# Optimization experiments

Hardware: AMD Instinct MI355X
Metric: run time of the kernel (lower is better)

## Reference

```python
import jax, jax.numpy as jnp
import numpy as np

M = 16384      # total flat points per role (8 scenes x 2048 pts)
D = 256        # d_model
H = 4          # heads
K = 16         # knn neighbors
DFF = 1024     # 4*D
LN_EPS = 1e-5


def _ln(x, g, b):
    m = jnp.mean(x, axis=-1, keepdims=True)
    v = jnp.mean((x - m) ** 2, axis=-1, keepdims=True)
    return (x - m) / jnp.sqrt(v + LN_EPS) * g + b


def _knn_block(x, coord, ctx, ctx_coord, idx,
               Wq, Wk, Wv, Wo, g1, b1, pe_w, pe_b,
               W1, bf1, W2, bf2, g2, b2):
    # x: [M,D] query feats; ctx: [N,D] context feats; idx: [M,K] neighbor ids (-1 = invalid)
    m, d = x.shape
    k = idx.shape[1]
    dh = d // H
    valid = idx >= 0
    idx_c = jnp.where(valid, idx, 0)

    xn = _ln(x, g1, b1)
    q = (xn @ Wq).reshape(m, H, dh)                      # [M,H,dh]
    k_all = ctx @ Wk                                     # [N,D]
    v_all = ctx @ Wv                                     # [N,D]

    rel = coord[:, None, :] - ctx_coord[idx_c]           # [M,K,3]
    pe = rel @ pe_w + pe_b                               # [M,K,D] relative position encoding
    kg = (k_all[idx_c] + pe).reshape(m, k, H, dh)        # gathered keys  [M,K,H,dh]
    vg = (v_all[idx_c] + pe).reshape(m, k, H, dh)        # gathered values

    scale = jnp.asarray(1.0 / np.sqrt(dh), x.dtype)
    scores = jnp.einsum('mhd,mkhd->mhk', q, kg) * scale
    scores = jnp.where(valid[:, None, :], scores, jnp.asarray(-1e9, x.dtype))
    attn = jax.nn.softmax(scores, axis=-1)
    out = jnp.einsum('mhk,mkhd->mhd', attn, vg).reshape(m, d) @ Wo
    x = x + out
    h = jax.nn.gelu(_ln(x, g2, b2) @ W1 + bf1)
    return x + (h @ W2 + bf2)


def setup_inputs() -> dict:
    key = jax.random.key(0)
    ks = jax.random.split(key, 24)
    s = 0.02
    nblk = 2  # [0]=self(a), [1]=cross(a,b)
    inp = {
        'feat_a': jax.random.normal(ks[0], (M, D), jnp.float32),
        'coord_a': jax.random.normal(ks[1], (M, 3), jnp.float32),
        'feat_b': jax.random.normal(ks[2], (M, D), jnp.float32),
        'coord_b': jax.random.normal(ks[3], (M, 3), jnp.float32),
        'Wq': jax.random.normal(ks[4], (nblk, D, D), jnp.float32) * s,
        'Wk': jax.random.normal(ks[5], (nblk, D, D), jnp.float32) * s,
        'Wv': jax.random.normal(ks[6], (nblk, D, D), jnp.float32) * s,
        'Wo': jax.random.normal(ks[7], (nblk, D, D), jnp.float32) * s,
        'ln1_g': jnp.ones((nblk, D), jnp.float32),
        'ln1_b': jnp.zeros((nblk, D), jnp.float32),
        'pe_w': jax.random.normal(ks[8], (nblk, 3, D), jnp.float32) * s,
        'pe_b': jnp.zeros((nblk, D), jnp.float32),
        'ffn_w1': jax.random.normal(ks[9], (nblk, D, DFF), jnp.float32) * s,
        'ffn_b1': jnp.zeros((nblk, DFF), jnp.float32),
        'ffn_w2': jax.random.normal(ks[10], (nblk, DFF, D), jnp.float32) * s,
        'ffn_b2': jnp.zeros((nblk, D), jnp.float32),
        'ln2_g': jnp.ones((nblk, D), jnp.float32),
        'ln2_b': jnp.zeros((nblk, D), jnp.float32),
        'knn_a2a': jax.random.randint(ks[11], (M, K), 0, M, jnp.int64 if jax.config.jax_enable_x64 else jnp.int32),
        'knn_a2b': jax.random.randint(ks[12], (M, K), 0, M, jnp.int64 if jax.config.jax_enable_x64 else jnp.int32),
    }
    return inp


def reference(feat_a, coord_a, feat_b, coord_b,
              Wq, Wk, Wv, Wo, ln1_g, ln1_b, pe_w, pe_b,
              ffn_w1, ffn_b1, ffn_w2, ffn_b2, ln2_g, ln2_b,
              knn_a2a, knn_a2b):
    def params(i):
        return (Wq[i], Wk[i], Wv[i], Wo[i], ln1_g[i], ln1_b[i], pe_w[i], pe_b[i],
                ffn_w1[i], ffn_b1[i], ffn_w2[i], ffn_b2[i], ln2_g[i], ln2_b[i])
    # layer 'self(a)': feat[a] = block(feat[a], coord[a], knn_indexes['a2a'])
    fa = _knn_block(feat_a, coord_a, feat_a, coord_a, knn_a2a, *params(0))
    # layer 'cross(a,b)': feat[a] = block(query=feat[a], context=feat[b], knn_indexes['a2b'])
    fa = _knn_block(fa, coord_a, feat_b, coord_b, knn_a2b, *params(1))
    return fa
```

## Files before the change

kernel.cpp:

```cpp
#include <hip/hip_runtime.h>
#include <hip/hip_bf16.h>
#include <stdint.h>

#define MM 16384
#define DD 256
#define HH 4
#define KK 16
#define DFF_ 1024

typedef __attribute__((ext_vector_type(8))) short bf16x8;
typedef __attribute__((ext_vector_type(16))) float f32x16;
typedef __attribute__((ext_vector_type(2))) float f32x2;

__device__ __forceinline__ unsigned short f2bf(float f) {
    unsigned u = __builtin_bit_cast(unsigned, f);
    unsigned r = u + 0x7fffu + ((u >> 16) & 1u);
    return (unsigned short)(r >> 16);
}
__device__ __forceinline__ float bf2f(unsigned short h) {
    unsigned u = ((unsigned)h) << 16;
    return __builtin_bit_cast(float, u);
}


__global__ __launch_bounds__(256) void prep_weights(
        const float* __restrict__ Wq, const float* __restrict__ Wk,
        const float* __restrict__ Wv, const float* __restrict__ Wo,
        const float* __restrict__ W1, const float* __restrict__ W2,
        unsigned short* __restrict__ wf) {
    int t = blockIdx.x * blockDim.x + threadIdx.x;
    const float* src; unsigned short* dst;
    int kd, nsrc, rem, blk, e, sect;
    if (t < 131072) { sect = 0; rem = t; blk = rem >> 16; e = rem & 65535;
        src = Wq; dst = wf + blk * 65536; kd = 256; nsrc = 256; }
    else if (t < 262144) { sect = 1; rem = t - 131072; blk = rem >> 16; e = rem & 65535;
        src = Wk; dst = wf + 131072 + blk * 131072; kd = 256; nsrc = 256; }
    else if (t < 393216) { sect = 2; rem = t - 262144; blk = rem >> 16; e = rem & 65535;
        src = Wv; dst = wf + 131072 + blk * 131072; kd = 256; nsrc = 256; }
    else if (t < 524288) { sect = 0; rem = t - 393216; blk = rem >> 16; e = rem & 65535;
        src = Wo; dst = wf + 393216 + blk * 65536; kd = 256; nsrc = 256; }
    else if (t < 1048576) { sect = 0; rem = t - 524288; blk = rem >> 18; e = rem & 262143;
        src = W1; dst = wf + 524288 + blk * 262144; kd = 256; nsrc = 1024; }
    else if (t < 1572864) { sect = 0; rem = t - 1048576; blk = rem >> 18; e = rem & 262143;
        src = W2; dst = wf + 1048576 + blk * 262144; kd = 1024; nsrc = 256; }
    else return;
    int k = e / nsrc;
    int n = e - k * nsrc;
    if (sect == 1) n = (n >> 2) * 8 + (n & 3);
    else if (sect == 2) n = (n >> 2) * 8 + 4 + (n & 3);
    float v = src[(size_t)blk * kd * nsrc + e];
    int off = ((n >> 5) * (kd >> 4) + (k >> 4)) * 512 + (((k >> 3) & 1) * 32 + (n & 31)) * 8 + (k & 7);
    dst[off] = f2bf(v);
}

__global__ __launch_bounds__(256) void ln_to_frag(
        const float* __restrict__ x, const float* __restrict__ g,
        const float* __restrict__ b, unsigned short* __restrict__ out,
        int apply_ln) {
    int wave = threadIdx.x >> 6, lane = threadIdx.x & 63;
    int m = blockIdx.x * 4 + wave;
    const float4 xv = reinterpret_cast<const float4*>(x + (size_t)m * DD)[lane];
    float vals[4] = {xv.x, xv.y, xv.z, xv.w};
    int k0 = lane * 4;
    if (apply_ln) {
        float s = vals[0] + vals[1] + vals[2] + vals[3];
        float sq = vals[0]*vals[0] + vals[1]*vals[1] + vals[2]*vals[2] + vals[3]*vals[3];
        for (int o = 32; o; o >>= 1) { s += __shfl_xor(s, o, 64); sq += __shfl_xor(sq, o, 64); }
        float mean = s * (1.0f / DD);
        float var = sq * (1.0f / DD) - mean * mean;
        float rs = rsqrtf(var + 1e-5f);
        #pragma unroll
        for (int c = 0; c < 4; ++c)
            vals[c] = (vals[c] - mean) * rs * g[k0 + c] + b[k0 + c];
    }
    int chunk = ((m >> 5) * (DD >> 4) + (k0 >> 4)) * 64 + ((k0 >> 3) & 1) * 32 + (m & 31);
    ushort4 o4 = make_ushort4(f2bf(vals[0]), f2bf(vals[1]), f2bf(vals[2]), f2bf(vals[3]));
    *reinterpret_cast<ushort4*>(out + (size_t)chunk * 8 + (k0 & 7)) = o4;
}

constexpr int GOUT_F32 = 0;
constexpr int GOUT_BF16 = 1;
constexpr int GOUT_GELU_FRAG = 2;

template <int KGH>
__device__ __forceinline__ void compute_tile(
        const bf16x8* __restrict__ a0, const bf16x8* __restrict__ a1,
        const bf16x8* __restrict__ b0, const bf16x8* __restrict__ b1,
        f32x16 acc[2][2]) {
    #pragma unroll 4
    for (int g = 0; g < KGH; ++g) {
        bf16x8 av0 = a0[g * 64];
        bf16x8 av1 = a1[g * 64];
        bf16x8 bv0 = b0[g * 64];
        bf16x8 bv1 = b1[g * 64];
        acc[0][0] = __builtin_amdgcn_mfma_f32_32x32x16_bf16(av0, bv0, acc[0][0], 0, 0, 0);
        acc[0][1] = __builtin_amdgcn_mfma_f32_32x32x16_bf16(av0, bv1, acc[0][1], 0, 0, 0);
        acc[1][0] = __builtin_amdgcn_mfma_f32_32x32x16_bf16(av1, bv0, acc[1][0], 0, 0, 0);
        acc[1][1] = __builtin_amdgcn_mfma_f32_32x32x16_bf16(av1, bv1, acc[1][1], 0, 0, 0);
    }
}

template <int KD, int NOUT, int SPLITK, int MODE, bool RESID, bool BIAS>
__global__ __launch_bounds__(SPLITK * 128) void gemm_frag(
        const bf16x8* __restrict__ A, const bf16x8* __restrict__ B,
        void* __restrict__ outp, const float* __restrict__ resid,
        const float* __restrict__ bias, int out_kd) {
    static_assert(MODE != GOUT_GELU_FRAG || SPLITK == 1, "gelu path is 2-wave only");
    constexpr int KG = KD / 16;
    constexpr int KGH = KG / SPLITK;
    __shared__ float lds[SPLITK == 2 ? 2 * 64 * 64 : 2 * 32 * 33];
    int wave = threadIdx.x >> 6, lane = threadIdx.x & 63;
    int mhalf = wave & 1;
    int khalf = (SPLITK == 2) ? (wave >> 1) : 0;
    int m0 = blockIdx.x * 128 + mhalf * 64;
    int n0 = blockIdx.y * 64;
    const bf16x8* a0 = A + ((size_t)(m0 >> 5) * KG + khalf * KGH) * 64 + lane;
    const bf16x8* a1 = a0 + (size_t)KG * 64;
    const bf16x8* b0 = B + ((size_t)(n0 >> 5) * KG + khalf * KGH) * 64 + lane;
    const bf16x8* b1 = b0 + (size_t)KG * 64;
    f32x16 acc[2][2] = {};
    compute_tile<KGH>(a0, a1, b0, b1, acc);
    int col = lane & 31, rq = (lane >> 5) * 4;
    if constexpr (SPLITK == 2) {
        if (khalf == 1) {
            #pragma unroll
            for (int i = 0; i < 2; ++i)
            #pragma unroll
            for (int j = 0; j < 2; ++j)
            #pragma unroll
            for (int r = 0; r < 16; ++r) {
                int row = (r & 3) + 8 * (r >> 2) + rq + i * 32;
                lds[mhalf * 4096 + row * 64 + j * 32 + col] = acc[i][j][r];
            }
        }
        __syncthreads();
        if (khalf == 1) return;
        #pragma unroll
        for (int i = 0; i < 2; ++i)
        #pragma unroll
        for (int j = 0; j < 2; ++j)
        #pragma unroll
        for (int r = 0; r < 16; ++r) {
            int row = (r & 3) + 8 * (r >> 2) + rq + i * 32;
            acc[i][j][r] += lds[mhalf * 4096 + row * 64 + j * 32 + col];
        }
    }
    if constexpr (MODE != GOUT_GELU_FRAG) {
        #pragma unroll
        for (int i = 0; i < 2; ++i)
        #pragma unroll
        for (int j = 0; j < 2; ++j) {
            #pragma unroll
            for (int r = 0; r < 16; ++r) {
                int row = (r & 3) + 8 * (r >> 2) + rq;
                int m = m0 + i * 32 + row;
                int n = n0 + j * 32 + col;
                float v = acc[i][j][r];
                if (BIAS) v += bias[n];
                if (RESID) v += resid[(size_t)m * NOUT + n];
                if (MODE == GOUT_F32) ((float*)outp)[(size_t)m * NOUT + n] = v;
                else ((unsigned short*)outp)[(size_t)m * NOUT + n] = f2bf(v);
            }
        }
    } else {
        float* wlds = &lds[wave * 1056];
        for (int i = 0; i < 2; ++i)
        for (int j = 0; j < 2; ++j) {
            #pragma unroll
            for (int r = 0; r < 16; ++r) {
                int row = (r & 3) + 8 * (r >> 2) + rq;
                int n = n0 + j * 32 + col;
                float v = acc[i][j][r] + bias[n];
                float arg = v * (1.5957691216f + 0.0713548163f * v * v);
                v = v * __frcp_rn(1.0f + __expf(-arg));
                wlds[row * 33 + col] = v;
            }
            #pragma unroll
            for (int it = 0; it < 2; ++it) {
                int task = lane + it * 64;
                int row = task >> 2, cc = task & 3;
                int m = m0 + i * 32 + row;
                int k = n0 + j * 32 + cc * 8;
                float* p = &wlds[row * 33 + cc * 8];
                unsigned short us[8];
                #pragma unroll
                for (int e = 0; e < 8; ++e) us[e] = f2bf(p[e]);
                int chunk = ((m >> 5) * (out_kd >> 4) + (k >> 4)) * 64 + ((k >> 3) & 1) * 32 + (m & 31);
                reinterpret_cast<uint4*>(outp)[chunk] = *reinterpret_cast<uint4*>(us);
            }
        }
    }
}

__global__ __launch_bounds__(256) void gemm_qkv(
        const bf16x8* __restrict__ Aq, const bf16x8* __restrict__ Akv,
        const bf16x8* __restrict__ Bq, const bf16x8* __restrict__ Bkv,
        unsigned short* __restrict__ qout, unsigned char* __restrict__ kvout) {
    constexpr int KG = 16, KGH = 8;
    __shared__ float lds[2 * 64 * 64];
    int wave = threadIdx.x >> 6, lane = threadIdx.x & 63;
    int mhalf = wave & 1, khalf = wave >> 1;
    int y = blockIdx.y;
    bool isQ = y < 4;
    const bf16x8* A = isQ ? Aq : Akv;
    const bf16x8* B = isQ ? Bq : Bkv;
    int n0 = (isQ ? y : y - 4) * 64;
    int m0 = blockIdx.x * 128 + mhalf * 64;
    const bf16x8* a0 = A + ((size_t)(m0 >> 5) * KG + khalf * KGH) * 64 + lane;
    const bf16x8* a1 = a0 + (size_t)KG * 64;
    const bf16x8* b0 = B + ((size_t)(n0 >> 5) * KG + khalf * KGH) * 64 + lane;
    const bf16x8* b1 = b0 + (size_t)KG * 64;
    f32x16 acc[2][2] = {};
    compute_tile<KGH>(a0, a1, b0, b1, acc);
    int col = lane & 31, rq = (lane >> 5) * 4;
    if (khalf == 1) {
        #pragma unroll
        for (int i = 0; i < 2; ++i)
        #pragma unroll
        for (int j = 0; j < 2; ++j)
        #pragma unroll
        for (int r = 0; r < 16; ++r) {
            int row = (r & 3) + 8 * (r >> 2) + rq + i * 32;
            lds[mhalf * 4096 + row * 64 + j * 32 + col] = acc[i][j][r];
        }
    }
    __syncthreads();
    if (khalf == 1) return;
    #pragma unroll
    for (int i = 0; i < 2; ++i)
    #pragma unroll
    for (int j = 0; j < 2; ++j)
    #pragma unroll
    for (int r = 0; r < 16; ++r) {
        int row = (r & 3) + 8 * (r >> 2) + rq;
        int m = m0 + i * 32 + row;
        int n = n0 + j * 32 + col;
        float v = acc[i][j][r] + lds[mhalf * 4096 + (row + i * 32) * 64 + j * 32 + col];
        if (isQ) qout[(size_t)m * 256 + n] = f2bf(v);
        else kvout[(size_t)m * 512 + n] =
            (unsigned char)(__builtin_amdgcn_cvt_pk_fp8_f32(v, v, 0, false) & 0xff);
    }
}

__global__ __launch_bounds__(256) void attn_kernel(
        const unsigned short* __restrict__ q, const unsigned char* __restrict__ kv,
        const float* __restrict__ coord, const float* __restrict__ ctx_coord,
        const int* __restrict__ knn,
        const float* __restrict__ pe_w, const float* __restrict__ pe_b,
        unsigned short* __restrict__ out_frag) {
    int wave = threadIdx.x >> 6, lane = threadIdx.x & 63;
    int m = blockIdx.x * 4 + wave;
    int s = lane & 15;
    int d0 = (lane >> 4) * 64 + s * 4;

    ushort4 qv4 = *reinterpret_cast<const ushort4*>(q + (size_t)m * DD + d0);
    float qx = bf2f(qv4.x), qy = bf2f(qv4.y), qz = bf2f(qv4.z), qw = bf2f(qv4.w);
    float4 pw0 = *reinterpret_cast<const float4*>(pe_w + d0);
    float4 pw1 = *reinterpret_cast<const float4*>(pe_w + DD + d0);
    float4 pw2 = *reinterpret_cast<const float4*>(pe_w + 2 * DD + d0);
    float4 pbv = *reinterpret_cast<const float4*>(pe_b + d0);

    float cx = coord[m * 3], cy = coord[m * 3 + 1], cz = coord[m * 3 + 2];
    int myidx = knn[(size_t)m * KK + s];
    int icm = myidx < 0 ? 0 : myidx;
    float rx = cx - ctx_coord[icm * 3];
    float ry = cy - ctx_coord[icm * 3 + 1];
    float rz = cz - ctx_coord[icm * 3 + 2];

    float t0 = qx * pw0.x + qy * pw0.y + qz * pw0.z + qw * pw0.w;
    float t1 = qx * pw1.x + qy * pw1.y + qz * pw1.z + qw * pw1.w;
    float t2 = qx * pw2.x + qy * pw2.y + qz * pw2.z + qw * pw2.w;
    float t3 = qx * pbv.x + qy * pbv.y + qz * pbv.z + qw * pbv.w;
    #pragma unroll
    for (int o = 1; o < 16; o <<= 1) {
        t0 += __shfl_xor(t0, o, 64);
        t1 += __shfl_xor(t1, o, 64);
        t2 += __shfl_xor(t2, o, 64);
        t3 += __shfl_xor(t3, o, 64);
    }

    float sc_own = 0.0f;
    unsigned vpk[KK];
    #pragma unroll
    for (int j = 0; j < KK; ++j) {
        int ij = __shfl(myidx, j, 64);
        int ic = ij < 0 ? 0 : ij;
        uint2 kvv = *reinterpret_cast<const uint2*>(kv + (size_t)ic * 512 + (d0 >> 2) * 8);
        vpk[j] = kvv.y;
        f32x2 k01 = __builtin_amdgcn_cvt_pk_f32_fp8(kvv.x, false);
        f32x2 k23 = __builtin_amdgcn_cvt_pk_f32_fp8(kvv.x, true);
        float p = qx * k01.x + qy * k01.y + qz * k23.x + qw * k23.y;
        p += __shfl_xor(p, 1, 64);
        p += __shfl_xor(p, 2, 64);
        p += __shfl_xor(p, 4, 64);
        p += __shfl_xor(p, 8, 64);
        sc_own = (j == s) ? p : sc_own;
    }
    float corr = rx * t0 + ry * t1 + rz * t2 + t3;
    sc_own = (myidx >= 0) ? (sc_own + corr) * 0.125f : -1e9f;

    float mx = sc_own;
    mx = fmaxf(mx, __shfl_xor(mx, 1, 64));
    mx = fmaxf(mx, __shfl_xor(mx, 2, 64));
    mx = fmaxf(mx, __shfl_xor(mx, 4, 64));
    mx = fmaxf(mx, __shfl_xor(mx, 8, 64));
    float e = __expf(sc_own - mx);
    float sum = e;
    sum += __shfl_xor(sum, 1, 64);
    sum += __shfl_xor(sum, 2, 64);
    sum += __shfl_xor(sum, 4, 64);
    sum += __shfl_xor(sum, 8, 64);
    float w_own = e * __frcp_rn(sum);

    float wrx = w_own * rx, wry = w_own * ry, wrz = w_own * rz;
    #pragma unroll
    for (int o = 1; o < 16; o <<= 1) {
        wrx += __shfl_xor(wrx, o, 64);
        wry += __shfl_xor(wry, o, 64);
        wrz += __shfl_xor(wrz, o, 64);
    }

    int gbase = lane & 48;
    float ax = 0.f, ay = 0.f, az = 0.f, aw = 0.f;
    #pragma unroll
    for (int j = 0; j < KK; ++j) {
        float wj = __shfl(w_own, gbase + j, 64);
        f32x2 v01 = __builtin_amdgcn_cvt_pk_f32_fp8(vpk[j], false);
        f32x2 v23 = __builtin_amdgcn_cvt_pk_f32_fp8(vpk[j], true);
        ax += wj * v01.x;
        ay += wj * v01.y;
        az += wj * v23.x;
        aw += wj * v23.y;
    }
    ax += wrx * pw0.x + wry * pw1.x + wrz * pw2.x + pbv.x;
    ay += wrx * pw0.y + wry * pw1.y + wrz * pw2.y + pbv.y;
    az += wrx * pw0.z + wry * pw1.z + wrz * pw2.z + pbv.z;
    aw += wrx * pw0.w + wry * pw1.w + wrz * pw2.w + pbv.w;

    ushort4 o4 = make_ushort4(f2bf(ax), f2bf(ay), f2bf(az), f2bf(aw));
    int chunk = ((m >> 5) * (DD >> 4) + (d0 >> 4)) * 64 + ((d0 >> 3) & 1) * 32 + (m & 31);
    *reinterpret_cast<ushort4*>(out_frag + (size_t)chunk * 8 + (d0 & 7)) = o4;
}

extern "C" void kernel_launch(void* const* d_in, const int* in_sizes, int n_in,
                              void* d_out, int out_size, void* d_ws, size_t ws_size,
                              hipStream_t stream) {
    const float* feat_a = (const float*)d_in[0];
    const float* coord_a = (const float*)d_in[1];
    const float* feat_b = (const float*)d_in[2];
    const float* coord_b = (const float*)d_in[3];
    const float* Wq = (const float*)d_in[4];
    const float* Wk = (const float*)d_in[5];
    const float* Wv = (const float*)d_in[6];
    const float* Wo = (const float*)d_in[7];
    const float* ln1_g = (const float*)d_in[8];
    const float* ln1_b = (const float*)d_in[9];
    const float* pe_w = (const float*)d_in[10];
    const float* pe_b = (const float*)d_in[11];
    const float* W1 = (const float*)d_in[12];
    const float* b1 = (const float*)d_in[13];
    const float* W2 = (const float*)d_in[14];
    const float* b2 = (const float*)d_in[15];
    const float* ln2_g = (const float*)d_in[16];
    const float* ln2_b = (const float*)d_in[17];
    const int* knn_a2a = (const int*)d_in[18];
    const int* knn_a2b = (const int*)d_in[19];

    char* ws = (char*)d_ws;
    unsigned short* wfrag = (unsigned short*)ws;
    float* xmid = (float*)(ws + (4ull << 20));
    float* xout0 = (float*)(ws + (20ull << 20));
    unsigned short* qbuf = (unsigned short*)(ws + (36ull << 20));
    unsigned char* kvbuf = (unsigned char*)(ws + (52ull << 20));
    unsigned short* xnf = (unsigned short*)(ws + (68ull << 20));
    unsigned short* ctxf = (unsigned short*)(ws + (76ull << 20));
    unsigned short* attnf = (unsigned short*)(ws + (84ull << 20));
    unsigned short* geluf = (unsigned short*)(ws + (36ull << 20));

    const unsigned short* WQF = wfrag;
    const unsigned short* KVF = wfrag + 131072;
    const unsigned short* WOF = wfrag + 393216;
    const unsigned short* W1F = wfrag + 524288;
    const unsigned short* W2F = wfrag + 1048576;

    prep_weights<<<(1572864 + 255) / 256, 256, 0, stream>>>(Wq, Wk, Wv, Wo, W1, W2, wfrag);

    for (int blk = 0; blk < 2; ++blk) {
        const float* x_in = blk ? xout0 : feat_a;
        const float* ctx = blk ? feat_b : feat_a;
        const float* ccrd = blk ? coord_b : coord_a;
        const int* knn = blk ? knn_a2b : knn_a2a;
        float* x_out_final = blk ? (float*)d_out : xout0;

        ln_to_frag<<<MM / 4, 256, 0, stream>>>(ctx, nullptr, nullptr, ctxf, 0);
        ln_to_frag<<<MM / 4, 256, 0, stream>>>(x_in, ln1_g + blk * DD, ln1_b + blk * DD, xnf, 1);

        gemm_qkv<<<dim3(MM / 128, 12), 256, 0, stream>>>(
            (const bf16x8*)xnf, (const bf16x8*)ctxf,
            (const bf16x8*)(WQF + blk * 65536), (const bf16x8*)(KVF + blk * 131072),
            qbuf, kvbuf);

        attn_kernel<<<MM / 4, 256, 0, stream>>>(qbuf, kvbuf, coord_a, ccrd, knn,
                                                pe_w + blk * 3 * DD, pe_b + blk * DD, attnf);

        gemm_frag<256, 256, 2, GOUT_F32, true, false><<<dim3(MM / 128, 4), 256, 0, stream>>>(
            (const bf16x8*)attnf, (const bf16x8*)(WOF + blk * 65536), xmid, x_in, nullptr, 0);

        ln_to_frag<<<MM / 4, 256, 0, stream>>>(xmid, ln2_g + blk * DD, ln2_b + blk * DD, xnf, 1);

        gemm_frag<256, 1024, 1, GOUT_GELU_FRAG, false, true><<<dim3(MM / 128, 16), 128, 0, stream>>>(
            (const bf16x8*)xnf, (const bf16x8*)(W1F + blk * 262144), geluf, nullptr,
            b1 + blk * DFF_, 1024);

        gemm_frag<1024, 256, 2, GOUT_F32, true, true><<<dim3(MM / 128, 4), 256, 0, stream>>>(
            (const bf16x8*)geluf, (const bf16x8*)(W2F + blk * 262144), x_out_final, xmid,
            b2 + blk * DD, 0);
    }
}
```

Baseline: 362.0 us.

## Stage GEMM tiles through double-buffered LDS with direct global-to-LDS loads

Replaces the per-wave direct global fragment loads in all GEMMs with a shared double-buffered LDS pipeline fed by global_load_lds. Each 4-wave workgroup cooperatively stages A and B chunks into LDS, so the B tile is loaded once per block instead of once per wave. The next chunk's loads overlap the MFMAs on the current one. The W1/GELU GEMM moves from 2 waves to 4 waves with split-K, and prep_weights swaps division for shifts. The cost is 48KB of LDS per block, which may reduce occupancy, plus a barrier on every chunk.

```diff
diff --git a/kernel.cpp b/kernel.cpp
--- a/kernel.cpp
+++ b/kernel.cpp
@@ -20,6 +20,12 @@
 __device__ __forceinline__ float bf2f(unsigned short h) {
     unsigned u = ((unsigned)h) << 16;
     return __builtin_bit_cast(float, u);
+}
+
+__device__ __forceinline__ void gload_lds16(const void* g, void* l) {
+    __builtin_amdgcn_global_load_lds(
+        (__attribute__((address_space(1))) void*)(void*)g,
+        (__attribute__((address_space(3))) void*)l, 16, 0, 0);
 }
 
 
@@ -30,25 +36,25 @@
         unsigned short* __restrict__ wf) {
     int t = blockIdx.x * blockDim.x + threadIdx.x;
     const float* src; unsigned short* dst;
-    int kd, nsrc, rem, blk, e, sect;
+    int kd, lg, rem, blk, e, sect;
     if (t < 131072) { sect = 0; rem = t; blk = rem >> 16; e = rem & 65535;
-        src = Wq; dst = wf + blk * 65536; kd = 256; nsrc = 256; }
+        src = Wq; dst = wf + blk * 65536; kd = 256; lg = 8; }
     else if (t < 262144) { sect = 1; rem = t - 131072; blk = rem >> 16; e = rem & 65535;
-        src = Wk; dst = wf + 131072 + blk * 131072; kd = 256; nsrc = 256; }
+        src = Wk; dst = wf + 131072 + blk * 131072; kd = 256; lg = 8; }
     else if (t < 393216) { sect = 2; rem = t - 262144; blk = rem >> 16; e = rem & 65535;
-        src = Wv; dst = wf + 131072 + blk * 131072; kd = 256; nsrc = 256; }
+        src = Wv; dst = wf + 131072 + blk * 131072; kd = 256; lg = 8; }
     else if (t < 524288) { sect = 0; rem = t - 393216; blk = rem >> 16; e = rem & 65535;
-        src = Wo; dst = wf + 393216 + blk * 65536; kd = 256; nsrc = 256; }
+        src = Wo; dst = wf + 393216 + blk * 65536; kd = 256; lg = 8; }
     else if (t < 1048576) { sect = 0; rem = t - 524288; blk = rem >> 18; e = rem & 262143;
-        src = W1; dst = wf + 524288 + blk * 262144; kd = 256; nsrc = 1024; }
+        src = W1; dst = wf + 524288 + blk * 262144; kd = 256; lg = 10; }
     else if (t < 1572864) { sect = 0; rem = t - 1048576; blk = rem >> 18; e = rem & 262143;
-        src = W2; dst = wf + 1048576 + blk * 262144; kd = 1024; nsrc = 256; }
+        src = W2; dst = wf + 1048576 + blk * 262144; kd = 1024; lg = 8; }
     else return;
-    int k = e / nsrc;
-    int n = e - k * nsrc;
+    int k = e >> lg;
+    int n = e & ((1 << lg) - 1);
     if (sect == 1) n = (n >> 2) * 8 + (n & 3);
     else if (sect == 2) n = (n >> 2) * 8 + 4 + (n & 3);
-    float v = src[(size_t)blk * kd * nsrc + e];
+    float v = src[(size_t)blk * kd * (1 << lg) + e];
     int off = ((n >> 5) * (kd >> 4) + (k >> 4)) * 512 + (((k >> 3) & 1) * 32 + (n & 31)) * 8 + (k & 7);
     dst[off] = f2bf(v);
 }
@@ -79,62 +85,64 @@
 }
 
 constexpr int GOUT_F32 = 0;
-constexpr int GOUT_BF16 = 1;
 constexpr int GOUT_GELU_FRAG = 2;
 
-template <int KGH>
-__device__ __forceinline__ void compute_tile(
-        const bf16x8* __restrict__ a0, const bf16x8* __restrict__ a1,
-        const bf16x8* __restrict__ b0, const bf16x8* __restrict__ b1,
-        f32x16 acc[2][2]) {
-    #pragma unroll 4
-    for (int g = 0; g < KGH; ++g) {
-        bf16x8 av0 = a0[g * 64];
-        bf16x8 av1 = a1[g * 64];
-        bf16x8 bv0 = b0[g * 64];
-        bf16x8 bv1 = b1[g * 64];
-        acc[0][0] = __builtin_amdgcn_mfma_f32_32x32x16_bf16(av0, bv0, acc[0][0], 0, 0, 0);
-        acc[0][1] = __builtin_amdgcn_mfma_f32_32x32x16_bf16(av0, bv1, acc[0][1], 0, 0, 0);
-        acc[1][0] = __builtin_amdgcn_mfma_f32_32x32x16_bf16(av1, bv0, acc[1][0], 0, 0, 0);
-        acc[1][1] = __builtin_amdgcn_mfma_f32_32x32x16_bf16(av1, bv1, acc[1][1], 0, 0, 0);
-    }
-}
-
-template <int KD, int NOUT, int SPLITK, int MODE, bool RESID, bool BIAS>
-__global__ __launch_bounds__(SPLITK * 128) void gemm_frag(
+template <int KG>
+__device__ __forceinline__ void lds_gemm_core(
+        const bf16x8* __restrict__ A, const bf16x8* __restrict__ B,
+        int m0wg, int n0, char* raw, int wave, int lane, f32x16 acc[2][2]) {
+    constexpr int C = KG / 4;
+    const int mh = wave & 1, kh = wave >> 1;
+    const int mrow = m0wg >> 5, nrow = n0 >> 5;
+    auto stage = [&](int c, int sel) {
+        char* base = raw + sel * 24576;
+        #pragma unroll
+        for (int s = 0; s < 6; ++s) {
+            int b = wave * 6 + s;
+            const bf16x8* src;
+            if (b < 16)
+                src = A + ((size_t)(mrow + (b >> 2)) * KG + c * 4 + (b & 3)) * 64 + lane;
+            else
+                src = B + ((size_t)(nrow + ((b - 16) >> 2)) * KG + c * 4 + ((b - 16) & 3)) * 64 + lane;
+            gload_lds16(src, base + b * 1024);
+        }
+    };
+    stage(0, 0);
+    for (int c = 0; c < C; ++c) {
+        __syncthreads();
+        if (c + 1 < C) stage(c + 1, (c + 1) & 1);
+        const char* base = raw + (c & 1) * 24576;
+        #pragma unroll
+        for (int t = 0; t < 2; ++t) {
+            int kg = kh * 2 + t;
+            bf16x8 av0 = *(const bf16x8*)(base + ((2 * mh + 0) * 4 + kg) * 1024 + lane * 16);
+            bf16x8 av1 = *(const bf16x8*)(base + ((2 * mh + 1) * 4 + kg) * 1024 + lane * 16);
+            bf16x8 bv0 = *(const bf16x8*)(base + 16384 + kg * 1024 + lane * 16);
+            bf16x8 bv1 = *(const bf16x8*)(base + 16384 + (4 + kg) * 1024 + lane * 16);
+            acc[0][0] = __builtin_amdgcn_mfma_f32_32x32x16_bf16(av0, bv0, acc[0][0], 0, 0, 0);
+            acc[0][1] = __builtin_amdgcn_mfma_f32_32x32x16_bf16(av0, bv1, acc[0][1], 0, 0, 0);
+            acc[1][0] = __builtin_amdgcn_mfma_f32_32x32x16_bf16(av1, bv0, acc[1][0], 0, 0, 0);
+            acc[1][1] = __builtin_amdgcn_mfma_f32_32x32x16_bf16(av1, bv1, acc[1][1], 0, 0, 0);
+        }
+    }
+    __syncthreads();
+}
+
+template <int KD, int NOUT, int MODE, bool RESID, bool BIAS>
+__global__ __launch_bounds__(256) void gemm_frag(
         const bf16x8* __restrict__ A, const bf16x8* __restrict__ B,
         void* __restrict__ outp, const float* __restrict__ resid,
         const float* __restrict__ bias, int out_kd) {
-    static_assert(MODE != GOUT_GELU_FRAG || SPLITK == 1, "gelu path is 2-wave only");
     constexpr int KG = KD / 16;
-    constexpr int KGH = KG / SPLITK;
-    __shared__ float lds[SPLITK == 2 ? 2 * 64 * 64 : 2 * 32 * 33];
+    __shared__ char raw[49152];
     int wave = threadIdx.x >> 6, lane = threadIdx.x & 63;
-    int mhalf = wave & 1;
-    int khalf = (SPLITK == 2) ? (wave >> 1) : 0;
-    int m0 = blockIdx.x * 128 + mhalf * 64;
+    int mh = wave & 1, kh = wave >> 1;
     int n0 = blockIdx.y * 64;
-    const bf16x8* a0 = A + ((size_t)(m0 >> 5) * KG + khalf * KGH) * 64 + lane;
-    const bf16x8* a1 = a0 + (size_t)KG * 64;
-    const bf16x8* b0 = B + ((size_t)(n0 >> 5) * KG + khalf * KGH) * 64 + lane;
-    const bf16x8* b1 = b0 + (size_t)KG * 64;
     f32x16 acc[2][2] = {};
-    compute_tile<KGH>(a0, a1, b0, b1, acc);
+    lds_gemm_core<KG>(A, B, blockIdx.x * 128, n0, raw, wave, lane, acc);
     int col = lane & 31, rq = (lane >> 5) * 4;
-    if constexpr (SPLITK == 2) {
-        if (khalf == 1) {
-            #pragma unroll
-            for (int i = 0; i < 2; ++i)
-            #pragma unroll
-            for (int j = 0; j < 2; ++j)
-            #pragma unroll
-            for (int r = 0; r < 16; ++r) {
-                int row = (r & 3) + 8 * (r >> 2) + rq + i * 32;
-                lds[mhalf * 4096 + row * 64 + j * 32 + col] = acc[i][j][r];
-            }
-        }
-        __syncthreads();
-        if (khalf == 1) return;
+    float* red = (float*)raw;
+    if (kh == 1) {
         #pragma unroll
         for (int i = 0; i < 2; ++i)
         #pragma unroll
@@ -142,10 +150,22 @@
         #pragma unroll
         for (int r = 0; r < 16; ++r) {
             int row = (r & 3) + 8 * (r >> 2) + rq + i * 32;
-            acc[i][j][r] += lds[mhalf * 4096 + row * 64 + j * 32 + col];
-        }
-    }
-    if constexpr (MODE != GOUT_GELU_FRAG) {
+            red[mh * 4096 + row * 64 + j * 32 + col] = acc[i][j][r];
+        }
+    }
+    __syncthreads();
+    if (kh == 1) return;
+    #pragma unroll
+    for (int i = 0; i < 2; ++i)
+    #pragma unroll
+    for (int j = 0; j < 2; ++j)
+    #pragma unroll
+    for (int r = 0; r < 16; ++r) {
+        int row = (r & 3) + 8 * (r >> 2) + rq + i * 32;
+        acc[i][j][r] += red[mh * 4096 + row * 64 + j * 32 + col];
+    }
+    int m0 = blockIdx.x * 128 + mh * 64;
+    if constexpr (MODE == GOUT_F32) {
         #pragma unroll
         for (int i = 0; i < 2; ++i)
         #pragma unroll
@@ -158,12 +178,11 @@
                 float v = acc[i][j][r];
                 if (BIAS) v += bias[n];
                 if (RESID) v += resid[(size_t)m * NOUT + n];
-                if (MODE == GOUT_F32) ((float*)outp)[(size_t)m * NOUT + n] = v;
-                else ((unsigned short*)outp)[(size_t)m * NOUT + n] = f2bf(v);
+                ((float*)outp)[(size_t)m * NOUT + n] = v;
             }
         }
     } else {
-        float* wlds = &lds[wave * 1056];
+        float* wlds = (float*)(raw + 32768) + mh * 1056;
         for (int i = 0; i < 2; ++i)
         for (int j = 0; j < 2; ++j) {
             #pragma unroll
@@ -196,24 +215,19 @@
         const bf16x8* __restrict__ Aq, const bf16x8* __restrict__ Akv,
         const bf16x8* __restrict__ Bq, const bf16x8* __restrict__ Bkv,
         unsigned short* __restrict__ qout, unsigned char* __restrict__ kvout) {
-    constexpr int KG = 16, KGH = 8;
-    __shared__ float lds[2 * 64 * 64];
+    __shared__ char raw[49152];
     int wave = threadIdx.x >> 6, lane = threadIdx.x & 63;
-    int mhalf = wave & 1, khalf = wave >> 1;
+    int mh = wave & 1, kh = wave >> 1;
     int y = blockIdx.y;
     bool isQ = y < 4;
     const bf16x8* A = isQ ? Aq : Akv;
     const bf16x8* B = isQ ? Bq : Bkv;
     int n0 = (isQ ? y : y - 4) * 64;
-    int m0 = blockIdx.x * 128 + mhalf * 64;
-    const bf16x8* a0 = A + ((size_t)(m0 >> 5) * KG + khalf * KGH) * 64 + lane;
-    const bf16x8* a1 = a0 + (size_t)KG * 64;
-    const bf16x8* b0 = B + ((size_t)(n0 >> 5) * KG + khalf * KGH) * 64 + lane;
-    const bf16x8* b1 = b0 + (size_t)KG * 64;
     f32x16 acc[2][2] = {};
-    compute_tile<KGH>(a0, a1, b0, b1, acc);
+    lds_gemm_core<16>(A, B, blockIdx.x * 128, n0, raw, wave, lane, acc);
     int col = lane & 31, rq = (lane >> 5) * 4;
-    if (khalf == 1) {
+    float* red = (float*)raw;
+    if (kh == 1) {
         #pragma unroll
         for (int i = 0; i < 2; ++i)
         #pragma unroll
@@ -221,11 +235,12 @@
         #pragma unroll
         for (int r = 0; r < 16; ++r) {
             int row = (r & 3) + 8 * (r >> 2) + rq + i * 32;
-            lds[mhalf * 4096 + row * 64 + j * 32 + col] = acc[i][j][r];
+            red[mh * 4096 + row * 64 + j * 32 + col] = acc[i][j][r];
         }
     }
     __syncthreads();
-    if (khalf == 1) return;
+    if (kh == 1) return;
+    int m0 = blockIdx.x * 128 + mh * 64;
     #pragma unroll
     for (int i = 0; i < 2; ++i)
     #pragma unroll
@@ -235,7 +250,7 @@
         int row = (r & 3) + 8 * (r >> 2) + rq;
         int m = m0 + i * 32 + row;
         int n = n0 + j * 32 + col;
-        float v = acc[i][j][r] + lds[mhalf * 4096 + (row + i * 32) * 64 + j * 32 + col];
+        float v = acc[i][j][r] + red[mh * 4096 + (row + i * 32) * 64 + j * 32 + col];
         if (isQ) qout[(size_t)m * 256 + n] = f2bf(v);
         else kvout[(size_t)m * 512 + n] =
             (unsigned char)(__builtin_amdgcn_cvt_pk_fp8_f32(v, v, 0, false) & 0xff);
@@ -403,16 +418,16 @@
         attn_kernel<<<MM / 4, 256, 0, stream>>>(qbuf, kvbuf, coord_a, ccrd, knn,
                                                 pe_w + blk * 3 * DD, pe_b + blk * DD, attnf);
 
-        gemm_frag<256, 256, 2, GOUT_F32, true, false><<<dim3(MM / 128, 4), 256, 0, stream>>>(
+        gemm_frag<256, 256, GOUT_F32, true, false><<<dim3(MM / 128, 4), 256, 0, stream>>>(
             (const bf16x8*)attnf, (const bf16x8*)(WOF + blk * 65536), xmid, x_in, nullptr, 0);
 
         ln_to_frag<<<MM / 4, 256, 0, stream>>>(xmid, ln2_g + blk * DD, ln2_b + blk * DD, xnf, 1);
 
-        gemm_frag<256, 1024, 1, GOUT_GELU_FRAG, false, true><<<dim3(MM / 128, 16), 128, 0, stream>>>(
+        gemm_frag<256, 1024, GOUT_GELU_FRAG, false, true><<<dim3(MM / 128, 16), 256, 0, stream>>>(
             (const bf16x8*)xnf, (const bf16x8*)(W1F + blk * 262144), geluf, nullptr,
             b1 + blk * DFF_, 1024);
 
-        gemm_frag<1024, 256, 2, GOUT_F32, true, true><<<dim3(MM / 128, 4), 256, 0, stream>>>(
+        gemm_frag<1024, 256, GOUT_F32, true, true><<<dim3(MM / 128, 4), 256, 0, stream>>>(
             (const bf16x8*)geluf, (const bf16x8*)(W2F + blk * 262144), x_out_final, xmid,
             b2 + blk * DD, 0);
     }
```

After: 372.3 us. 1.03x slower.

## Replace split-K GEMM waves with 2x2 output tiling per block

Applied to the files above, without the earlier changes.

The GEMM kernels drop the split-K scheme, where two waves each reduced half of K and combined partial sums through LDS with a barrier. Instead each of four waves computes a distinct 64x64 output tile covering the full K range, so a block now covers 128x128 outputs and the grids are halved. This removes the LDS reduction, the barrier and the idle-wave epilogue, and gives A/B tiles more reuse across waves. The cost is fewer blocks and a longer serial K loop per wave, which may reduce latency hiding. The weight-prep kernel also replaces division with shifts.

```diff
diff --git a/kernel.cpp b/kernel.cpp
--- a/kernel.cpp
+++ b/kernel.cpp
@@ -30,25 +30,25 @@
         unsigned short* __restrict__ wf) {
     int t = blockIdx.x * blockDim.x + threadIdx.x;
     const float* src; unsigned short* dst;
-    int kd, nsrc, rem, blk, e, sect;
+    int kd, lg, rem, blk, e, sect;
     if (t < 131072) { sect = 0; rem = t; blk = rem >> 16; e = rem & 65535;
-        src = Wq; dst = wf + blk * 65536; kd = 256; nsrc = 256; }
+        src = Wq; dst = wf + blk * 65536; kd = 256; lg = 8; }
     else if (t < 262144) { sect = 1; rem = t - 131072; blk = rem >> 16; e = rem & 65535;
-        src = Wk; dst = wf + 131072 + blk * 131072; kd = 256; nsrc = 256; }
+        src = Wk; dst = wf + 131072 + blk * 131072; kd = 256; lg = 8; }
     else if (t < 393216) { sect = 2; rem = t - 262144; blk = rem >> 16; e = rem & 65535;
-        src = Wv; dst = wf + 131072 + blk * 131072; kd = 256; nsrc = 256; }
+        src = Wv; dst = wf + 131072 + blk * 131072; kd = 256; lg = 8; }
     else if (t < 524288) { sect = 0; rem = t - 393216; blk = rem >> 16; e = rem & 65535;
-        src = Wo; dst = wf + 393216 + blk * 65536; kd = 256; nsrc = 256; }
+        src = Wo; dst = wf + 393216 + blk * 65536; kd = 256; lg = 8; }
     else if (t < 1048576) { sect = 0; rem = t - 524288; blk = rem >> 18; e = rem & 262143;
-        src = W1; dst = wf + 524288 + blk * 262144; kd = 256; nsrc = 1024; }
+        src = W1; dst = wf + 524288 + blk * 262144; kd = 256; lg = 10; }
     else if (t < 1572864) { sect = 0; rem = t - 1048576; blk = rem >> 18; e = rem & 262143;
-        src = W2; dst = wf + 1048576 + blk * 262144; kd = 1024; nsrc = 256; }
+        src = W2; dst = wf + 1048576 + blk * 262144; kd = 1024; lg = 8; }
     else return;
-    int k = e / nsrc;
-    int n = e - k * nsrc;
+    int k = e >> lg;
+    int n = e & ((1 << lg) - 1);
     if (sect == 1) n = (n >> 2) * 8 + (n & 3);
     else if (sect == 2) n = (n >> 2) * 8 + 4 + (n & 3);
-    float v = src[(size_t)blk * kd * nsrc + e];
+    float v = src[(size_t)blk * kd * (1 << lg) + e];
     int off = ((n >> 5) * (kd >> 4) + (k >> 4)) * 512 + (((k >> 3) & 1) * 32 + (n & 31)) * 8 + (k & 7);
     dst[off] = f2bf(v);
 }
@@ -79,16 +79,15 @@
 }
 
 constexpr int GOUT_F32 = 0;
-constexpr int GOUT_BF16 = 1;
 constexpr int GOUT_GELU_FRAG = 2;
 
-template <int KGH>
+template <int KG>
 __device__ __forceinline__ void compute_tile(
         const bf16x8* __restrict__ a0, const bf16x8* __restrict__ a1,
         const bf16x8* __restrict__ b0, const bf16x8* __restrict__ b1,
         f32x16 acc[2][2]) {
     #pragma unroll 4
-    for (int g = 0; g < KGH; ++g) {
+    for (int g = 0; g < KG; ++g) {
         bf16x8 av0 = a0[g * 64];
         bf16x8 av1 = a1[g * 64];
         bf16x8 bv0 = b0[g * 64];
@@ -100,52 +99,25 @@
     }
 }
 
-template <int KD, int NOUT, int SPLITK, int MODE, bool RESID, bool BIAS>
-__global__ __launch_bounds__(SPLITK * 128) void gemm_frag(
+template <int KD, int NOUT, int MODE, bool RESID, bool BIAS>
+__global__ __launch_bounds__(256) void gemm_frag(
         const bf16x8* __restrict__ A, const bf16x8* __restrict__ B,
         void* __restrict__ outp, const float* __restrict__ resid,
         const float* __restrict__ bias, int out_kd) {
-    static_assert(MODE != GOUT_GELU_FRAG || SPLITK == 1, "gelu path is 2-wave only");
     constexpr int KG = KD / 16;
-    constexpr int KGH = KG / SPLITK;
-    __shared__ float lds[SPLITK == 2 ? 2 * 64 * 64 : 2 * 32 * 33];
+    __shared__ float lds[MODE == GOUT_GELU_FRAG ? 4 * 1056 : 4];
     int wave = threadIdx.x >> 6, lane = threadIdx.x & 63;
-    int mhalf = wave & 1;
-    int khalf = (SPLITK == 2) ? (wave >> 1) : 0;
-    int m0 = blockIdx.x * 128 + mhalf * 64;
-    int n0 = blockIdx.y * 64;
-    const bf16x8* a0 = A + ((size_t)(m0 >> 5) * KG + khalf * KGH) * 64 + lane;
+    int wm = wave & 1, wn = wave >> 1;
+    int m0 = blockIdx.x * 128 + wm * 64;
+    int n0 = blockIdx.y * 128 + wn * 64;
+    const bf16x8* a0 = A + ((size_t)(m0 >> 5) * KG) * 64 + lane;
     const bf16x8* a1 = a0 + (size_t)KG * 64;
-    const bf16x8* b0 = B + ((size_t)(n0 >> 5) * KG + khalf * KGH) * 64 + lane;
+    const bf16x8* b0 = B + ((size_t)(n0 >> 5) * KG) * 64 + lane;
     const bf16x8* b1 = b0 + (size_t)KG * 64;
     f32x16 acc[2][2] = {};
-    compute_tile<KGH>(a0, a1, b0, b1, acc);
+    compute_tile<KG>(a0, a1, b0, b1, acc);
     int col = lane & 31, rq = (lane >> 5) * 4;
-    if constexpr (SPLITK == 2) {
-        if (khalf == 1) {
-            #pragma unroll
-            for (int i = 0; i < 2; ++i)
-            #pragma unroll
-            for (int j = 0; j < 2; ++j)
-            #pragma unroll
-            for (int r = 0; r < 16; ++r) {
-                int row = (r & 3) + 8 * (r >> 2) + rq + i * 32;
-                lds[mhalf * 4096 + row * 64 + j * 32 + col] = acc[i][j][r];
-            }
-        }
-        __syncthreads();
-        if (khalf == 1) return;
-        #pragma unroll
-        for (int i = 0; i < 2; ++i)
-        #pragma unroll
-        for (int j = 0; j < 2; ++j)
-        #pragma unroll
-        for (int r = 0; r < 16; ++r) {
-            int row = (r & 3) + 8 * (r >> 2) + rq + i * 32;
-            acc[i][j][r] += lds[mhalf * 4096 + row * 64 + j * 32 + col];
-        }
-    }
-    if constexpr (MODE != GOUT_GELU_FRAG) {
+    if constexpr (MODE == GOUT_F32) {
         #pragma unroll
         for (int i = 0; i < 2; ++i)
         #pragma unroll
@@ -158,8 +130,7 @@
                 float v = acc[i][j][r];
                 if (BIAS) v += bias[n];
                 if (RESID) v += resid[(size_t)m * NOUT + n];
-                if (MODE == GOUT_F32) ((float*)outp)[(size_t)m * NOUT + n] = v;
-                else ((unsigned short*)outp)[(size_t)m * NOUT + n] = f2bf(v);
+                ((float*)outp)[(size_t)m * NOUT + n] = v;
             }
         }
     } else {
@@ -196,36 +167,22 @@
         const bf16x8* __restrict__ Aq, const bf16x8* __restrict__ Akv,
         const bf16x8* __restrict__ Bq, const bf16x8* __restrict__ Bkv,
         unsigned short* __restrict__ qout, unsigned char* __restrict__ kvout) {
-    constexpr int KG = 16, KGH = 8;
-    __shared__ float lds[2 * 64 * 64];
+    constexpr int KG = 16;
     int wave = threadIdx.x >> 6, lane = threadIdx.x & 63;
-    int mhalf = wave & 1, khalf = wave >> 1;
+    int wm = wave & 1, wn = wave >> 1;
     int y = blockIdx.y;
-    bool isQ = y < 4;
+    bool isQ = y < 2;
     const bf16x8* A = isQ ? Aq : Akv;
     const bf16x8* B = isQ ? Bq : Bkv;
-    int n0 = (isQ ? y : y - 4) * 64;
-    int m0 = blockIdx.x * 128 + mhalf * 64;
-    const bf16x8* a0 = A + ((size_t)(m0 >> 5) * KG + khalf * KGH) * 64 + lane;
+    int n0 = (isQ ? y : y - 2) * 128 + wn * 64;
+    int m0 = blockIdx.x * 128 + wm * 64;
+    const bf16x8* a0 = A + ((size_t)(m0 >> 5) * KG) * 64 + lane;
     const bf16x8* a1 = a0 + (size_t)KG * 64;
-    const bf16x8* b0 = B + ((size_t)(n0 >> 5) * KG + khalf * KGH) * 64 + lane;
+    const bf16x8* b0 = B + ((size_t)(n0 >> 5) * KG) * 64 + lane;
     const bf16x8* b1 = b0 + (size_t)KG * 64;
     f32x16 acc[2][2] = {};
-    compute_tile<KGH>(a0, a1, b0, b1, acc);
+    compute_tile<KG>(a0, a1, b0, b1, acc);
     int col = lane & 31, rq = (lane >> 5) * 4;
-    if (khalf == 1) {
-        #pragma unroll
-        for (int i = 0; i < 2; ++i)
-        #pragma unroll
-        for (int j = 0; j < 2; ++j)
-        #pragma unroll
-        for (int r = 0; r < 16; ++r) {
-            int row = (r & 3) + 8 * (r >> 2) + rq + i * 32;
-            lds[mhalf * 4096 + row * 64 + j * 32 + col] = acc[i][j][r];
-        }
-    }
-    __syncthreads();
-    if (khalf == 1) return;
     #pragma unroll
     for (int i = 0; i < 2; ++i)
     #pragma unroll
@@ -235,7 +192,7 @@
         int row = (r & 3) + 8 * (r >> 2) + rq;
         int m = m0 + i * 32 + row;
         int n = n0 + j * 32 + col;
-        float v = acc[i][j][r] + lds[mhalf * 4096 + (row + i * 32) * 64 + j * 32 + col];
+        float v = acc[i][j][r];
         if (isQ) qout[(size_t)m * 256 + n] = f2bf(v);
         else kvout[(size_t)m * 512 + n] =
             (unsigned char)(__builtin_amdgcn_cvt_pk_fp8_f32(v, v, 0, false) & 0xff);
@@ -395,7 +352,7 @@
         ln_to_frag<<<MM / 4, 256, 0, stream>>>(ctx, nullptr, nullptr, ctxf, 0);
         ln_to_frag<<<MM / 4, 256, 0, stream>>>(x_in, ln1_g + blk * DD, ln1_b + blk * DD, xnf, 1);
 
-        gemm_qkv<<<dim3(MM / 128, 12), 256, 0, stream>>>(
+        gemm_qkv<<<dim3(MM / 128, 6), 256, 0, stream>>>(
             (const bf16x8*)xnf, (const bf16x8*)ctxf,
             (const bf16x8*)(WQF + blk * 65536), (const bf16x8*)(KVF + blk * 131072),
             qbuf, kvbuf);
@@ -403,16 +360,16 @@
         attn_kernel<<<MM / 4, 256, 0, stream>>>(qbuf, kvbuf, coord_a, ccrd, knn,
                                                 pe_w + blk * 3 * DD, pe_b + blk * DD, attnf);
 
-        gemm_frag<256, 256, 2, GOUT_F32, true, false><<<dim3(MM / 128, 4), 256, 0, stream>>>(
+        gemm_frag<256, 256, GOUT_F32, true, false><<<dim3(MM / 128, 2), 256, 0, stream>>>(
             (const bf16x8*)attnf, (const bf16x8*)(WOF + blk * 65536), xmid, x_in, nullptr, 0);
 
         ln_to_frag<<<MM / 4, 256, 0, stream>>>(xmid, ln2_g + blk * DD, ln2_b + blk * DD, xnf, 1);
 
-        gemm_frag<256, 1024, 1, GOUT_GELU_FRAG, false, true><<<dim3(MM / 128, 16), 128, 0, stream>>>(
+        gemm_frag<256, 1024, GOUT_GELU_FRAG, false, true><<<dim3(MM / 128, 8), 256, 0, stream>>>(
             (const bf16x8*)xnf, (const bf16x8*)(W1F + blk * 262144), geluf, nullptr,
             b1 + blk * DFF_, 1024);
 
-        gemm_frag<1024, 256, 2, GOUT_F32, true, true><<<dim3(MM / 128, 4), 256, 0, stream>>>(
+        gemm_frag<1024, 256, GOUT_F32, true, true><<<dim3(MM / 128, 2), 256, 0, stream>>>(
             (const bf16x8*)geluf, (const bf16x8*)(W2F + blk * 262144), x_out_final, xmid,
             b2 + blk * DD, 0);
     }
```

Result: faster. 349.7 us (-3.4%).
